# Kernel tuning notes

Measured on AMD Instinct MI355X. Metric: run time of the kernel, lower is better.

The kernel has to match this reference:

```python
import jax, jax.numpy as jnp
import numpy as np

NUM_HEADS = 5
TEMP = 0.3
NEG_FILL = -1e-7  # note: NOT -inf; masked entries still contribute ~exp(0) to softmax, faithful to torch code


def setup_inputs() -> dict:
    key = jax.random.key(0)
    k1, k2, k3, k4, k5 = jax.random.split(key, 5)
    B, N, F_IN, F_OUT = 8, 1024, 320, 320
    h = jax.random.normal(k1, (B, N, F_IN), dtype=jnp.float32)
    Wqk = jax.random.normal(k2, (F_IN, 2 * F_IN), dtype=jnp.float32) * (1.0 / np.sqrt(F_IN))
    bqk = jax.random.normal(k3, (2 * F_IN,), dtype=jnp.float32) * 0.01
    weight = jax.random.normal(k4, (F_IN, F_OUT), dtype=jnp.float32) * (1.0 / np.sqrt(F_OUT))
    bias = jax.random.normal(k5, (F_OUT,), dtype=jnp.float32) * 0.01
    return {"h": h, "Wqk": Wqk, "bqk": bqk, "weight": weight, "bias": bias}


def reference(h, Wqk, bqk, weight, bias):
    B, N, F = h.shape
    H = NUM_HEADS
    D = F // H
    # linear -> [b, n, 2F]; einops 'b n (h d qk)' => reshape (b, n, h, d, 2)
    qk = (h @ Wqk + bqk).reshape(B, N, H, D, 2)
    q = jnp.transpose(qk[..., 0], (0, 2, 1, 3))  # b h n d
    k = jnp.transpose(qk[..., 1], (0, 2, 1, 3))  # b h n d
    scale = D ** -0.5
    dots = jnp.einsum('bhqd,bhkd->bhqk', q, k) * scale  # b h n n
    at = dots.sum(axis=1)  # b n n  (sum over heads)
    # sort-based threshold: keep values >= descending-sorted value at index N//6
    thr = jax.lax.top_k(at, N // 6 + 1)[0][..., -1]  # b n
    adj = jnp.where(at < thr[:, :, None], jnp.asarray(NEG_FILL, at.dtype), at)
    attn = jax.nn.softmax(adj / TEMP, axis=2)  # b n n
    out_feature = jnp.einsum('bij,bjd->bid', attn, h)  # values = raw input h
    return out_feature @ weight + bias
```

## Files before the change

### kernel.cpp

```cpp
#include <hip/hip_runtime.h>
#include <hip/hip_fp16.h>


typedef __attribute__((ext_vector_type(8))) _Float16 half8;
typedef __attribute__((ext_vector_type(4))) float f32x4;

__device__ __forceinline__ void stage_tile(const __half* g, __half* lds,
                                           int nrow16, int ld, int wave, int lane) {
    const int r = lane >> 2;
    const int c = ((lane & 3) ^ ((lane >> 3) & 3)) * 8;
    for (int i = wave; i < nrow16; i += 4) {
        const __half* src = g + (long)(i * 16 + r) * ld + c;
        __builtin_amdgcn_global_load_lds(
            (const __attribute__((address_space(1))) unsigned int*)src,
            (__attribute__((address_space(3))) unsigned int*)(lds + i * 512),
            16, 0, 0);
    }
}

template <int WM, int WN, int EPI>
__global__ __launch_bounds__(256) void gemm_nt(
    const __half* __restrict__ A, const __half* __restrict__ B,
    void* __restrict__ C, void* __restrict__ C2,
    const float* __restrict__ bias,
    int K, int lda, int ldb, int ldc,
    long sA, long sB, long sC, float alpha)
{
    constexpr int BM = WM * 64;
    constexpr int BN = WN * 64;
    __shared__ __half smem[BM * 32 + BN * 32];
    __half* sA_ = smem;
    __half* sB_ = smem + BM * 32;

    const int tid  = threadIdx.x;
    const int lane = tid & 63;
    const int wave = tid >> 6;
    const int wm   = wave / WN;
    const int wn   = wave % WN;
    const int bz   = blockIdx.z;

    const __half* Ab = A + bz * sA + (long)blockIdx.y * BM * lda;
    const __half* Bb = B + bz * sB + (long)blockIdx.x * BN * ldb;

    f32x4 acc[4][4];
    #pragma unroll
    for (int i = 0; i < 4; ++i)
        #pragma unroll
        for (int j = 0; j < 4; ++j) acc[i][j] = (f32x4){0.f, 0.f, 0.f, 0.f};

    const int lrow = lane & 15;
    const int quad = lane >> 4;
    const int swz = (quad ^ ((lrow >> 1) & 3)) * 8;

    for (int k0 = 0; k0 < K; k0 += 32) {
        stage_tile(Ab + k0, sA_, BM / 16, lda, wave, lane);
        stage_tile(Bb + k0, sB_, BN / 16, ldb, wave, lane);
        __syncthreads();

        const __half* pA = sA_ + (wm * 64 + lrow) * 32 + swz;
        const __half* pB = sB_ + (wn * 64 + lrow) * 32 + swz;
        half8 ah[4], bh[4];
        #pragma unroll
        for (int mt = 0; mt < 4; ++mt) ah[mt] = *(const half8*)(pA + mt * 512);
        #pragma unroll
        for (int nt = 0; nt < 4; ++nt) bh[nt] = *(const half8*)(pB + nt * 512);
        #pragma unroll
        for (int mt = 0; mt < 4; ++mt)
            #pragma unroll
            for (int nt = 0; nt < 4; ++nt)
                acc[mt][nt] = __builtin_amdgcn_mfma_f32_16x16x32_f16(
                    ah[mt], bh[nt], acc[mt][nt], 0, 0, 0);
        __syncthreads();
    }

    const int row_base = blockIdx.y * BM + wm * 64;
    const int col_base = blockIdx.x * BN + wn * 64;
    #pragma unroll
    for (int mt = 0; mt < 4; ++mt)
        #pragma unroll
        for (int nt = 0; nt < 4; ++nt)
            #pragma unroll
            for (int r = 0; r < 4; ++r) {
                const int row = row_base + mt * 16 + quad * 4 + r;
                const int col = col_base + nt * 16 + lrow;
                const float v = acc[mt][nt][r];
                if (EPI == 1) {
                    const float val = v + bias[col];
                    const long idx = (long)row * 320 + (col >> 1);
                    if (col & 1) ((__half*)C2)[idx] = __float2half(val);
                    else         ((__half*)C)[idx]  = __float2half(val);
                } else if (EPI == 2) {
                    ((__half*)C)[(long)row * ldc + col] = __float2half(v);
                } else if (EPI == 3) {
                    ((float*)C)[bz * sC + (long)row * ldc + col] = v + bias[col];
                } else {
                    ((__half*)C)[bz * sC + (long)row * ldc + col] =
                        __float2half(alpha * v);
                }
            }
}

__global__ __launch_bounds__(256) void conv_f16(const float4* __restrict__ src,
                                                ushort4* __restrict__ dst)
{
    const int i = blockIdx.x * 256 + threadIdx.x;
    const float4 v = src[i];
    ushort4 o;
    o.x = __half_as_ushort(__float2half(v.x));
    o.y = __half_as_ushort(__float2half(v.y));
    o.z = __half_as_ushort(__float2half(v.z));
    o.w = __half_as_ushort(__float2half(v.w));
    dst[i] = o;
}

__global__ __launch_bounds__(256) void transpose_f16(
    const float* __restrict__ src, __half* __restrict__ dst, int ldS, int ldT)
{
    __shared__ float t[32][33];
    const int c0 = blockIdx.x * 32, r0 = blockIdx.y * 32;
    const int lx = threadIdx.x & 31, ly = threadIdx.x >> 5;
    #pragma unroll
    for (int i = 0; i < 4; ++i)
        t[ly + 8 * i][lx] = src[(long)(r0 + ly + 8 * i) * ldS + c0 + lx];
    __syncthreads();
    #pragma unroll
    for (int i = 0; i < 4; ++i)
        dst[(long)(c0 + ly + 8 * i) * ldT + r0 + lx] = __float2half(t[lx][ly + 8 * i]);
}

__global__ __launch_bounds__(256) void topk_softmax(const __half* __restrict__ at,
                                                    __half* __restrict__ attn)
{
    __shared__ int hist[4][256];
    const int lane = threadIdx.x & 63;
    const int wave = threadIdx.x >> 6;
    const long row = (long)blockIdx.x * 4 + wave;

    unsigned short vs[16];
    {
        const uint4* p = (const uint4*)(at + row * 1024 + lane * 16);
        *(uint4*)&vs[0] = p[0];
        *(uint4*)&vs[8] = p[1];
    }

    unsigned key[16];
    #pragma unroll
    for (int i = 0; i < 16; ++i) {
        const unsigned u = vs[i];
        key[i] = (u & 0x8000u) ? ((~u) & 0xFFFFu) : (u | 0x8000u);
    }

    unsigned prefix = 0, pmask = 0;
    int kk = 171;

    #pragma unroll
    for (int pass = 0; pass < 2; ++pass) {
        const int shift = 8 - 8 * pass;
        *(int4*)&hist[wave][lane * 4] = make_int4(0, 0, 0, 0);
        __syncthreads();
        #pragma unroll
        for (int i = 0; i < 16; ++i) {
            if ((key[i] & pmask) == prefix)
                atomicAdd(&hist[wave][(key[i] >> shift) & 255], 1);
        }
        __syncthreads();
        const int4 hh = *(const int4*)&hist[wave][lane * 4];
        const int s = hh.x + hh.y + hh.z + hh.w;
        int suf = s;
        #pragma unroll
        for (int off = 1; off < 64; off <<= 1) {
            const int o = __shfl_down(suf, off);
            if (lane + off < 64) suf += o;
        }
        const int cgt3 = suf - s;
        const int cgt2 = cgt3 + hh.w;
        const int cgt1 = cgt2 + hh.z;
        const int cgt0 = cgt1 + hh.y;
        int pick = 0x7FFFFFFF;
        if (cgt3 < kk && kk <= cgt3 + hh.w) pick = ((4 * lane + 3) << 16) | (kk - cgt3);
        if (cgt2 < kk && kk <= cgt2 + hh.z) pick = ((4 * lane + 2) << 16) | (kk - cgt2);
        if (cgt1 < kk && kk <= cgt1 + hh.y) pick = ((4 * lane + 1) << 16) | (kk - cgt1);
        if (cgt0 < kk && kk <= cgt0 + hh.x) pick = ((4 * lane + 0) << 16) | (kk - cgt0);
        #pragma unroll
        for (int off = 32; off > 0; off >>= 1) pick = min(pick, __shfl_xor(pick, off));
        const unsigned digit = (unsigned)(pick >> 16);
        kk = pick & 0xFFFF;
        prefix |= digit << shift;
        pmask  |= 0xFFu << shift;
        if (pass == 0) __syncthreads();
    }

    const unsigned short tu = (prefix & 0x8000u) ? (unsigned short)(prefix & 0x7FFFu)
                                                 : (unsigned short)((~prefix) & 0xFFFFu);
    const float thr = __half2float(__ushort_as_half(tu));

    float lg[16];
    float mx = -3.4e38f;
    #pragma unroll
    for (int i = 0; i < 16; ++i) {
        const float v = __half2float(__ushort_as_half(vs[i]));
        const float a = (v < thr) ? -1e-7f : v;
        lg[i] = a * (1.0f / 0.3f);
        mx = fmaxf(mx, lg[i]);
    }
    #pragma unroll
    for (int off = 32; off > 0; off >>= 1) mx = fmaxf(mx, __shfl_xor(mx, off));

    float e[16];
    float sum = 0.f;
    #pragma unroll
    for (int i = 0; i < 16; ++i) { e[i] = __expf(lg[i] - mx); sum += e[i]; }
    #pragma unroll
    for (int off = 32; off > 0; off >>= 1) sum += __shfl_xor(sum, off);
    const float inv = 1.0f / sum;

    unsigned short os[16];
    #pragma unroll
    for (int i = 0; i < 16; ++i) os[i] = __half_as_ushort(__float2half(e[i] * inv));
    uint4* q = (uint4*)(attn + row * 1024 + lane * 16);
    q[0] = *(const uint4*)&os[0];
    q[1] = *(const uint4*)&os[8];
}

extern "C" void kernel_launch(void* const* d_in, const int* in_sizes, int n_in,
                              void* d_out, int out_size, void* d_ws, size_t ws_size,
                              hipStream_t stream) {
    (void)in_sizes; (void)n_in; (void)out_size; (void)ws_size;

    const float* h      = (const float*)d_in[0];
    const float* Wqk    = (const float*)d_in[1];
    const float* bqk    = (const float*)d_in[2];
    const float* weight = (const float*)d_in[3];
    const float* bias   = (const float*)d_in[4];
    float* out = (float*)d_out;

    char* p = (char*)d_ws;
    __half* at   = (__half*)p; p += 8388608L * 2;
    __half* attn = (__half*)p; p += 8388608L * 2;
    __half* h16  = (__half*)p; p += 2621440L * 2;
    __half* Q    = (__half*)p; p += 2621440L * 2;
    __half* Kb   = (__half*)p; p += 2621440L * 2;
    __half* WqkT = (__half*)p; p += 640L * 320 * 2;
    __half* wTp  = (__half*)p; p += 384L * 320 * 2;
    __half* hWT  = (__half*)p; p += 384L * 8192 * 2;

    conv_f16<<<2560, 256, 0, stream>>>((const float4*)h, (ushort4*)h16);
    transpose_f16<<<dim3(20, 10, 1), 256, 0, stream>>>(Wqk, WqkT, 640, 320);
    transpose_f16<<<dim3(10, 10, 1), 256, 0, stream>>>(weight, wTp, 320, 320);

    gemm_nt<2, 2, 2><<<dim3(64, 3, 1), 256, 0, stream>>>(
        wTp, h16, hWT, nullptr, nullptr,
        320, 320, 320, 8192, 0, 0, 0, 1.0f);

    gemm_nt<4, 1, 1><<<dim3(10, 32, 1), 256, 0, stream>>>(
        h16, WqkT, Q, Kb, bqk,
        320, 320, 320, 0, 0, 0, 0, 1.0f);

    gemm_nt<2, 2, 4><<<dim3(8, 8, 8), 256, 0, stream>>>(
        Q, Kb, at, nullptr, nullptr,
        320, 320, 320, 1024, 327680, 327680, 1048576, 0.125f);

    topk_softmax<<<2048, 256, 0, stream>>>(at, attn);

    gemm_nt<4, 1, 3><<<dim3(5, 4, 8), 256, 0, stream>>>(
        attn, hWT, out, nullptr, bias,
        1024, 1024, 8192, 320, 1048576, 1024, 327680, 1.0f);
}
```

Measured before the change: 156.7 us.

## Double-buffer GEMM LDS tiles and fuse prep kernels into one launch

The GEMM main loop now uses two LDS buffers. The next K-tile's global-to-LDS load is issued before the MFMAs on the current tile, and one of the two barriers per iteration is removed. This is meant to overlap memory latency with compute, at the cost of doubling shared memory per block, which may reduce occupancy. Separately, the fp16 conversion and the two weight-transpose kernels are merged into a single launch to cut launch overhead.

```diff
diff --git a/kernel.cpp b/kernel.cpp
--- a/kernel.cpp
+++ b/kernel.cpp
@@ -28,9 +28,8 @@
 {
     constexpr int BM = WM * 64;
     constexpr int BN = WN * 64;
-    __shared__ __half smem[BM * 32 + BN * 32];
-    __half* sA_ = smem;
-    __half* sB_ = smem + BM * 32;
+    constexpr int BUF = BM * 32 + BN * 32;
+    __shared__ __half smem[2 * BUF];
 
     const int tid  = threadIdx.x;
     const int lane = tid & 63;
@@ -52,13 +51,24 @@
     const int quad = lane >> 4;
     const int swz = (quad ^ ((lrow >> 1) & 3)) * 8;
 
-    for (int k0 = 0; k0 < K; k0 += 32) {
-        stage_tile(Ab + k0, sA_, BM / 16, lda, wave, lane);
-        stage_tile(Bb + k0, sB_, BN / 16, ldb, wave, lane);
+    const int nIter = K >> 5;
+
+    stage_tile(Ab, smem, BM / 16, lda, wave, lane);
+    stage_tile(Bb, smem + BM * 32, BN / 16, ldb, wave, lane);
+
+    for (int it = 0; it < nIter; ++it) {
         __syncthreads();
 
-        const __half* pA = sA_ + (wm * 64 + lrow) * 32 + swz;
-        const __half* pB = sB_ + (wn * 64 + lrow) * 32 + swz;
+        if (it + 1 < nIter) {
+            __half* nb = smem + ((it + 1) & 1) * BUF;
+            const int k1 = (it + 1) << 5;
+            stage_tile(Ab + k1, nb, BM / 16, lda, wave, lane);
+            stage_tile(Bb + k1, nb + BM * 32, BN / 16, ldb, wave, lane);
+        }
+
+        const __half* buf = smem + (it & 1) * BUF;
+        const __half* pA = buf + (wm * 64 + lrow) * 32 + swz;
+        const __half* pB = buf + BM * 32 + (wn * 64 + lrow) * 32 + swz;
         half8 ah[4], bh[4];
         #pragma unroll
         for (int mt = 0; mt < 4; ++mt) ah[mt] = *(const half8*)(pA + mt * 512);
@@ -70,7 +80,6 @@
             for (int nt = 0; nt < 4; ++nt)
                 acc[mt][nt] = __builtin_amdgcn_mfma_f32_16x16x32_f16(
                     ah[mt], bh[nt], acc[mt][nt], 0, 0, 0);
-        __syncthreads();
     }
 
     const int row_base = blockIdx.y * BM + wm * 64;
@@ -100,24 +109,36 @@
             }
 }
 
-__global__ __launch_bounds__(256) void conv_f16(const float4* __restrict__ src,
-                                                ushort4* __restrict__ dst)
+__global__ __launch_bounds__(256) void prep_all(
+    const float* __restrict__ h, ushort4* __restrict__ h16,
+    const float* __restrict__ Wqk, __half* __restrict__ WqkT,
+    const float* __restrict__ weight, __half* __restrict__ wTp)
 {
-    const int i = blockIdx.x * 256 + threadIdx.x;
-    const float4 v = src[i];
-    ushort4 o;
-    o.x = __half_as_ushort(__float2half(v.x));
-    o.y = __half_as_ushort(__float2half(v.y));
-    o.z = __half_as_ushort(__float2half(v.z));
-    o.w = __half_as_ushort(__float2half(v.w));
-    dst[i] = o;
-}
-
-__global__ __launch_bounds__(256) void transpose_f16(
-    const float* __restrict__ src, __half* __restrict__ dst, int ldS, int ldT)
-{
+    const int bx = blockIdx.x;
+    if (bx < 2560) {
+        const int i = bx * 256 + threadIdx.x;
+        const float4 v = ((const float4*)h)[i];
+        ushort4 o;
+        o.x = __half_as_ushort(__float2half(v.x));
+        o.y = __half_as_ushort(__float2half(v.y));
+        o.z = __half_as_ushort(__float2half(v.z));
+        o.w = __half_as_ushort(__float2half(v.w));
+        h16[i] = o;
+        return;
+    }
     __shared__ float t[32][33];
-    const int c0 = blockIdx.x * 32, r0 = blockIdx.y * 32;
+    const float* src;
+    __half* dst;
+    int ldS, ldT, c0, r0;
+    if (bx < 2760) {
+        const int b = bx - 2560;
+        src = Wqk; dst = WqkT; ldS = 640; ldT = 320;
+        c0 = (b % 20) * 32; r0 = (b / 20) * 32;
+    } else {
+        const int b = bx - 2760;
+        src = weight; dst = wTp; ldS = 320; ldT = 320;
+        c0 = (b % 10) * 32; r0 = (b / 10) * 32;
+    }
     const int lx = threadIdx.x & 31, ly = threadIdx.x >> 5;
     #pragma unroll
     for (int i = 0; i < 4; ++i)
@@ -244,9 +265,7 @@
     __half* wTp  = (__half*)p; p += 384L * 320 * 2;
     __half* hWT  = (__half*)p; p += 384L * 8192 * 2;
 
-    conv_f16<<<2560, 256, 0, stream>>>((const float4*)h, (ushort4*)h16);
-    transpose_f16<<<dim3(20, 10, 1), 256, 0, stream>>>(Wqk, WqkT, 640, 320);
-    transpose_f16<<<dim3(10, 10, 1), 256, 0, stream>>>(weight, wTp, 320, 320);
+    prep_all<<<2860, 256, 0, stream>>>(h, (ushort4*)h16, Wqk, WqkT, weight, wTp);
 
     gemm_nt<2, 2, 2><<<dim3(64, 3, 1), 256, 0, stream>>>(
         wTp, h16, hWT, nullptr, nullptr,
```

Result: faster. 146.0 us (-6.8%).
